# Kernel tuning notes

Hardware: AMD Instinct MI355X
Metric: run time of the kernel (lower is better)

Reference implementation:

```python
import jax, jax.numpy as jnp
import numpy as np

NUM_CLASSES = 32
N = 2_000_000
EPS = jnp.float32(np.finfo(np.float32).eps)  # torch.finfo(torch.float32).eps


def setup_inputs() -> dict:
    key = jax.random.key(0)
    k1, k2 = jax.random.split(key)
    y_true = jax.random.normal(k1, (N, NUM_CLASSES), dtype=jnp.float32)
    y_pred = jax.random.normal(k2, (N, NUM_CLASSES), dtype=jnp.float32)
    confusion_matrix = jnp.zeros((NUM_CLASSES, NUM_CLASSES), dtype=jnp.float32)
    return {"y_true": y_true, "y_pred": y_pred, "confusion_matrix": confusion_matrix}


def reference(y_true, y_pred, confusion_matrix):
    C = confusion_matrix.shape[0]
    # update(): argmax then scatter-accumulate into the confusion matrix
    t = jnp.argmax(y_true, axis=1)  # [N] int
    p = jnp.argmax(y_pred, axis=1)  # [N] int
    flat = t * C + p                # flattened (row, col) index
    hist = jnp.zeros((C * C,), dtype=jnp.float32).at[flat].add(1.0)
    cm = confusion_matrix + hist.reshape(C, C)
    # compute() with average='macro'
    tp = jnp.diag(cm)
    predicted_positives = jnp.sum(cm, axis=0)
    precision_per_class = tp / (predicted_positives + EPS)
    return jnp.mean(precision_per_class)
```

## Files before the change

kernel.cpp:

```cpp
#include <hip/hip_runtime.h>

#define C 32
#define BINS (C * C)
#define FLT_EPS 1.1920928955078125e-07f

__global__ __launch_bounds__(256) void hist_kernel(
    const float* __restrict__ yt,
    const float* __restrict__ yp,
    unsigned int* __restrict__ ghist,
    int N)
{
    __shared__ unsigned int lhist[BINS];
    const int tid = threadIdx.x;
    for (int i = tid; i < BINS; i += blockDim.x) lhist[i] = 0u;
    __syncthreads();

    const int lane8 = tid & 7;
    const int rowInBlock = tid >> 3;
    const int rowsPerIter = (gridDim.x * blockDim.x) >> 3;
    int row = blockIdx.x * (blockDim.x >> 3) + rowInBlock;

    for (; row < N; row += rowsPerIter) {
        const float4 a = ((const float4*)(yt + (size_t)row * C))[lane8];
        const float4 b = ((const float4*)(yp + (size_t)row * C))[lane8];

        const int base = lane8 * 4;
        float tv = a.x; int ti = base;
        if (a.y > tv) { tv = a.y; ti = base + 1; }
        if (a.z > tv) { tv = a.z; ti = base + 2; }
        if (a.w > tv) { tv = a.w; ti = base + 3; }
        float pv = b.x; int pi = base;
        if (b.y > pv) { pv = b.y; pi = base + 1; }
        if (b.z > pv) { pv = b.z; pi = base + 2; }
        if (b.w > pv) { pv = b.w; pi = base + 3; }

        #pragma unroll
        for (int m = 1; m < 8; m <<= 1) {
            float otv = __shfl_xor(tv, m);
            int   oti = __shfl_xor(ti, m);
            if (otv > tv || (otv == tv && oti < ti)) { tv = otv; ti = oti; }
            float opv = __shfl_xor(pv, m);
            int   opi = __shfl_xor(pi, m);
            if (opv > pv || (opv == pv && opi < pi)) { pv = opv; pi = opi; }
        }

        if (lane8 == 0) {
            atomicAdd(&lhist[ti * C + pi], 1u);
        }
    }

    __syncthreads();
    for (int i = tid; i < BINS; i += blockDim.x) {
        unsigned int v = lhist[i];
        if (v) atomicAdd(&ghist[i], v);
    }
}

__global__ __launch_bounds__(64) void finalize_kernel(
    const unsigned int* __restrict__ ghist,
    const float* __restrict__ cm_in,
    float* __restrict__ out)
{
    const int j = threadIdx.x;
    float prec = 0.0f;
    if (j < C) {
        float pp = 0.0f;
        #pragma unroll
        for (int i = 0; i < C; ++i) {
            pp += (float)ghist[i * C + j] + cm_in[i * C + j];
        }
        float tp = (float)ghist[j * C + j] + cm_in[j * C + j];
        prec = tp / (pp + FLT_EPS);
    }
    #pragma unroll
    for (int m = 1; m < 32; m <<= 1) {
        prec += __shfl_xor(prec, m);
    }
    if (j == 0) out[0] = prec / (float)C;
}

extern "C" void kernel_launch(void* const* d_in, const int* in_sizes, int n_in,
                              void* d_out, int out_size, void* d_ws, size_t ws_size,
                              hipStream_t stream)
{
    const float* yt = (const float*)d_in[0];
    const float* yp = (const float*)d_in[1];
    const float* cm = (const float*)d_in[2];
    float* out = (float*)d_out;
    const int N = in_sizes[0] / C;

    unsigned int* ghist = (unsigned int*)d_ws;
    hipMemsetAsync(ghist, 0, BINS * sizeof(unsigned int), stream);

    hist_kernel<<<1024, 256, 0, stream>>>(yt, yp, ghist, N);
    finalize_kernel<<<1, 64, 0, stream>>>(ghist, cm, out);
}
```

Baseline: 487.1 us.

## Stage row tiles through LDS and write per-block partials instead of global atomics

Each block now loads 256-row tiles of y_true and y_pred into padded shared memory with nontemporal vector loads, and one thread per row does a serial argmax, replacing the shuffle-based 8-lane reduction. Instead of atomically merging full histograms into global memory (which needed a memset), each block writes only column sums and the diagonal to a per-block partial buffer, reduced by a 1024-thread finalize kernel. This removes the memset launch and the global atomics, but adds several __syncthreads per tile and serializes the two input loads, which may cut memory-level parallelism on a bandwidth-bound kernel.

```diff
diff --git a/kernel.cpp b/kernel.cpp
--- a/kernel.cpp
+++ b/kernel.cpp
@@ -2,81 +2,136 @@
 
 #define C 32
 #define BINS (C * C)
+#define TILE_ROWS 256
+#define ROWPAD 36
+#define NBLOCKS 1024
 #define FLT_EPS 1.1920928955078125e-07f
+
+typedef float v4f __attribute__((ext_vector_type(4)));
 
 __global__ __launch_bounds__(256) void hist_kernel(
     const float* __restrict__ yt,
     const float* __restrict__ yp,
-    unsigned int* __restrict__ ghist,
+    unsigned int* __restrict__ partial,
     int N)
 {
+    __shared__ float buf[TILE_ROWS * ROWPAD];
     __shared__ unsigned int lhist[BINS];
-    const int tid = threadIdx.x;
-    for (int i = tid; i < BINS; i += blockDim.x) lhist[i] = 0u;
-    __syncthreads();
+    const int t = threadIdx.x;
+    for (int i = t; i < BINS; i += 256) lhist[i] = 0u;
 
-    const int lane8 = tid & 7;
-    const int rowInBlock = tid >> 3;
-    const int rowsPerIter = (gridDim.x * blockDim.x) >> 3;
-    int row = blockIdx.x * (blockDim.x >> 3) + rowInBlock;
+    const int numTiles = (N + TILE_ROWS - 1) / TILE_ROWS;
+    int ti_reg = 0;
 
-    for (; row < N; row += rowsPerIter) {
-        const float4 a = ((const float4*)(yt + (size_t)row * C))[lane8];
-        const float4 b = ((const float4*)(yp + (size_t)row * C))[lane8];
+    for (int tile = blockIdx.x; tile < numTiles; tile += gridDim.x) {
+        const size_t row0 = (size_t)tile * TILE_ROWS;
+        const int rowsValid = min(TILE_ROWS, N - (int)row0);
 
-        const int base = lane8 * 4;
-        float tv = a.x; int ti = base;
-        if (a.y > tv) { tv = a.y; ti = base + 1; }
-        if (a.z > tv) { tv = a.z; ti = base + 2; }
-        if (a.w > tv) { tv = a.w; ti = base + 3; }
-        float pv = b.x; int pi = base;
-        if (b.y > pv) { pv = b.y; pi = base + 1; }
-        if (b.z > pv) { pv = b.z; pi = base + 2; }
-        if (b.w > pv) { pv = b.w; pi = base + 3; }
+        {
+            const v4f* src = (const v4f*)(yt + row0 * C);
+            #pragma unroll
+            for (int q = 0; q < 8; ++q) {
+                const int lin = q * 256 + t;
+                const int r = lin >> 3, m = lin & 7;
+                if (r < rowsValid) {
+                    v4f v = __builtin_nontemporal_load(src + lin);
+                    *(v4f*)&buf[r * ROWPAD + m * 4] = v;
+                }
+            }
+        }
+        __syncthreads();
+        if (t < rowsValid) {
+            float bv = -__builtin_inff(); int bi = C;
+            const float* rowp = &buf[t * ROWPAD];
+            #pragma unroll
+            for (int j = 0; j < C; ++j) {
+                const int c = (j + t) & (C - 1);
+                const float v = rowp[c];
+                const bool better = (v > bv) || (v == bv && c < bi);
+                bv = better ? v : bv;
+                bi = better ? c : bi;
+            }
+            ti_reg = bi;
+        }
+        __syncthreads();
 
-        #pragma unroll
-        for (int m = 1; m < 8; m <<= 1) {
-            float otv = __shfl_xor(tv, m);
-            int   oti = __shfl_xor(ti, m);
-            if (otv > tv || (otv == tv && oti < ti)) { tv = otv; ti = oti; }
-            float opv = __shfl_xor(pv, m);
-            int   opi = __shfl_xor(pi, m);
-            if (opv > pv || (opv == pv && opi < pi)) { pv = opv; pi = opi; }
+        {
+            const v4f* src = (const v4f*)(yp + row0 * C);
+            #pragma unroll
+            for (int q = 0; q < 8; ++q) {
+                const int lin = q * 256 + t;
+                const int r = lin >> 3, m = lin & 7;
+                if (r < rowsValid) {
+                    v4f v = __builtin_nontemporal_load(src + lin);
+                    *(v4f*)&buf[r * ROWPAD + m * 4] = v;
+                }
+            }
         }
-
-        if (lane8 == 0) {
-            atomicAdd(&lhist[ti * C + pi], 1u);
+        __syncthreads();
+        if (t < rowsValid) {
+            float bv = -__builtin_inff(); int bi = C;
+            const float* rowp = &buf[t * ROWPAD];
+            #pragma unroll
+            for (int j = 0; j < C; ++j) {
+                const int c = (j + t) & (C - 1);
+                const float v = rowp[c];
+                const bool better = (v > bv) || (v == bv && c < bi);
+                bv = better ? v : bv;
+                bi = better ? c : bi;
+            }
+            atomicAdd(&lhist[ti_reg * C + bi], 1u);
         }
+        __syncthreads();
     }
 
-    __syncthreads();
-    for (int i = tid; i < BINS; i += blockDim.x) {
-        unsigned int v = lhist[i];
-        if (v) atomicAdd(&ghist[i], v);
+    if (t < C) {
+        unsigned int cs = 0;
+        #pragma unroll
+        for (int i = 0; i < C; ++i) cs += lhist[i * C + t];
+        partial[(size_t)blockIdx.x * 64 + t] = cs;
+        partial[(size_t)blockIdx.x * 64 + C + t] = lhist[t * C + t];
     }
 }
 
-__global__ __launch_bounds__(64) void finalize_kernel(
-    const unsigned int* __restrict__ ghist,
+__global__ __launch_bounds__(1024) void finalize_kernel(
+    const unsigned int* __restrict__ partial,
     const float* __restrict__ cm_in,
     float* __restrict__ out)
 {
-    const int j = threadIdx.x;
-    float prec = 0.0f;
-    if (j < C) {
-        float pp = 0.0f;
+    __shared__ float sums[16][64];
+    const int tid = threadIdx.x;
+    const int col = tid & 63;
+    const int kg = tid >> 6;
+
+    unsigned int s = 0;
+    #pragma unroll 8
+    for (int k = kg * (NBLOCKS / 16); k < (kg + 1) * (NBLOCKS / 16); ++k)
+        s += partial[(size_t)k * 64 + col];
+    sums[kg][col] = (float)s;
+    __syncthreads();
+
+    if (tid < 64) {
+        float tot = 0.0f;
         #pragma unroll
-        for (int i = 0; i < C; ++i) {
-            pp += (float)ghist[i * C + j] + cm_in[i * C + j];
-        }
-        float tp = (float)ghist[j * C + j] + cm_in[j * C + j];
-        prec = tp / (pp + FLT_EPS);
+        for (int g = 0; g < 16; ++g) tot += sums[g][tid];
+        sums[0][tid] = tot;
     }
-    #pragma unroll
-    for (int m = 1; m < 32; m <<= 1) {
-        prec += __shfl_xor(prec, m);
+    __syncthreads();
+
+    if (tid < C) {
+        const int j = tid;
+        float pp = sums[0][j];
+        float tp = sums[0][C + j];
+        float cmcol = 0.0f;
+        #pragma unroll
+        for (int i = 0; i < C; ++i) cmcol += cm_in[i * C + j];
+        pp += cmcol;
+        tp += cm_in[j * C + j];
+        float prec = tp / (pp + FLT_EPS);
+        #pragma unroll
+        for (int m = 1; m < C; m <<= 1) prec += __shfl_xor(prec, m);
+        if (j == 0) out[0] = prec * (1.0f / (float)C);
     }
-    if (j == 0) out[0] = prec / (float)C;
 }
 
 extern "C" void kernel_launch(void* const* d_in, const int* in_sizes, int n_in,
@@ -89,9 +144,8 @@
     float* out = (float*)d_out;
     const int N = in_sizes[0] / C;
 
-    unsigned int* ghist = (unsigned int*)d_ws;
-    hipMemsetAsync(ghist, 0, BINS * sizeof(unsigned int), stream);
+    unsigned int* partial = (unsigned int*)d_ws;
 
-    hist_kernel<<<1024, 256, 0, stream>>>(yt, yp, ghist, N);
-    finalize_kernel<<<1, 64, 0, stream>>>(ghist, cm, out);
+    hist_kernel<<<NBLOCKS, 256, 0, stream>>>(yt, yp, partial, N);
+    finalize_kernel<<<1, 1024, 0, stream>>>(partial, cm, out);
 }
```

Result: no change. 480.5 us (-1.4%).
